# Kernel tuning notes

Measured on AMD Instinct MI355X. Metric: run time of the kernel, lower is better.

The kernel has to match this reference:

```python
import jax, jax.numpy as jnp
import numpy as np

NI = 256  # channels (c)
EPS = 1e-5  # BatchNorm eps


def setup_inputs() -> dict:
    key = jax.random.key(0)
    ks = jax.random.split(key, 7)
    n, c, h, w = 8, NI, 96, 96
    inp = jax.random.normal(ks[0], (n, c, h, w), dtype=jnp.float32)
    bn_gamma = jnp.ones((c,), dtype=jnp.float32)
    bn_beta = jnp.zeros((c,), dtype=jnp.float32)
    s_qkv = 1.0 / np.sqrt(c)
    w_qkv = jax.random.uniform(ks[1], (c, 3 * c), dtype=jnp.float32, minval=-s_qkv, maxval=s_qkv)
    b_qkv = jax.random.uniform(ks[2], (3 * c,), dtype=jnp.float32, minval=-s_qkv, maxval=s_qkv)
    w_proj = jax.random.uniform(ks[3], (c, c), dtype=jnp.float32, minval=-s_qkv, maxval=s_qkv)
    b_proj = jax.random.uniform(ks[4], (c,), dtype=jnp.float32, minval=-s_qkv, maxval=s_qkv)
    return {"inp": inp, "bn_gamma": bn_gamma, "bn_beta": bn_beta,
            "w_qkv": w_qkv, "b_qkv": b_qkv, "w_proj": w_proj, "b_proj": b_proj}


def reference(inp, bn_gamma, bn_beta, w_qkv, b_qkv, w_proj, b_proj):
    n, c, h, w = inp.shape
    # BatchNorm2d (training-mode batch statistics, biased variance)
    mean = jnp.mean(inp, axis=(0, 2, 3), keepdims=True)
    var = jnp.var(inp, axis=(0, 2, 3), keepdims=True)
    xn = (inp - mean) * jax.lax.rsqrt(var + EPS)
    xn = xn * bn_gamma.reshape(1, c, 1, 1) + bn_beta.reshape(1, c, 1, 1)
    # (n, c, h*w) -> (n, s, c)
    x = jnp.transpose(xn.reshape(n, c, h * w), (0, 2, 1))
    # fused QKV projection: (n, s, 3c)
    qkv = x @ w_qkv + b_qkv
    q, k, v = jnp.split(qkv, 3, axis=-1)  # each (n, s, c); nheads=1
    # linear attention: v + q @ (k^T @ v), avoids the (s, s) score matrix
    kv = jnp.einsum('nsd,nse->nde', k, v)        # (n, c, c)
    attn = v + jnp.einsum('nsd,nde->nse', q, kv)  # (n, s, c)
    # output projection (dropout is identity in eval mode)
    y = attn @ w_proj + b_proj                    # (n, s, c)
    y = jnp.transpose(y, (0, 2, 1)).reshape(n, c, h, w)
    return y + inp
```

## Files before the change

kernel.cpp:

```cpp
#include <hip/hip_runtime.h>
#include <hip/hip_bf16.h>
#include <stdint.h>

#define S 9216
#define C 256
#define NB 8
#define EPS 1e-5f
#define LDST 40
#define GSPL 18
#define GLD 144

typedef __attribute__((ext_vector_type(8))) short bf16x8;
typedef __attribute__((ext_vector_type(4))) float f32x4;
typedef unsigned short u16;
typedef unsigned int u32;

#define WS_SC   0
#define WS_RX   4096
#define WS_DS   16384
#define WS_U    20480
#define WS_PV   32768
#define WS_P1   45056
#define WS_CZ   49152
#define WS_WKT  65536
#define WS_WPT  196608
#define WS_WPV  327680
#define WS_GB   458752
#define WS_T1   1507328
#define WS_AC2  2555904
#define WS_M    3604480
#define WS_P    4718592

__device__ __forceinline__ float bf2f(u16 b) { return __uint_as_float((u32)b << 16); }
__device__ __forceinline__ u16 cvt1(float x) {
    __hip_bfloat16 h = __float2bfloat16(x);
    return *(u16*)&h;
}
__device__ __forceinline__ bf16x8 pack8(float4 a, float4 b) {
    union { bf16x8 v; u16 h[8]; } u;
    u.h[0] = cvt1(a.x); u.h[1] = cvt1(a.y); u.h[2] = cvt1(a.z); u.h[3] = cvt1(a.w);
    u.h[4] = cvt1(b.x); u.h[5] = cvt1(b.y); u.h[6] = cvt1(b.z); u.h[7] = cvt1(b.w);
    return u.v;
}
__device__ __forceinline__ void tile_enum(int tile, int& ti, int& tj) {
    if (tile < 4) { ti = tile; tj = tile; }
    else {
        const int u = tile - 4;
        ti = (u < 3) ? 0 : ((u < 5) ? 1 : 2);
        tj = (u < 3) ? (u + 1) : ((u < 5) ? (u - 1) : 3);
    }
}

__global__ __launch_bounds__(256)
void wt_build(const float* __restrict__ w_qkv, const float* __restrict__ w_proj,
              u16* __restrict__ wkT, u16* __restrict__ wpT) {
    const int r0 = blockIdx.x, c = threadIdx.x;
    if (r0 < 256) {
        wkT[(size_t)r0 * 256 + c] = cvt1(w_qkv[(size_t)c * 768 + 256 + r0]);
    } else {
        const int o = r0 - 256;
        wpT[(size_t)o * 256 + c] = cvt1(w_proj[(size_t)c * 256 + o]);
    }
}

__global__ __launch_bounds__(256)
void wpv_gemm(const u16* __restrict__ wpT, const float* __restrict__ w_qkv,
              u16* __restrict__ Wpv) {
    const int bid = blockIdx.x;
    const int ot = bid >> 2, ct = bid & 3;
    const int tid = threadIdx.x;
    const int w = tid >> 6, l = tid & 63, g = l >> 4, r = l & 15;
    const int wr = w >> 1, wc = w & 1;
    const int mb = ot * 64 + wr * 32, nb = ct * 64 + wc * 32;

    f32x4 acc[2][2];
    #pragma unroll
    for (int i = 0; i < 2; ++i)
        #pragma unroll
        for (int j = 0; j < 2; ++j) acc[i][j] = (f32x4){0.f, 0.f, 0.f, 0.f};

    for (int k0 = 0; k0 < 256; k0 += 32) {
        bf16x8 a[2], b[2];
        #pragma unroll
        for (int i = 0; i < 2; ++i)
            a[i] = *(const bf16x8*)&wpT[(size_t)(mb + i * 16 + r) * 256 + k0 + g * 8];
        #pragma unroll
        for (int j = 0; j < 2; ++j) {
            const float* p = w_qkv + (size_t)(nb + j * 16 + r) * 768 + 512 + k0 + g * 8;
            b[j] = pack8(*(const float4*)p, *(const float4*)(p + 4));
        }
        #pragma unroll
        for (int i = 0; i < 2; ++i)
            #pragma unroll
            for (int j = 0; j < 2; ++j)
                acc[i][j] = __builtin_amdgcn_mfma_f32_16x16x32_bf16(a[i], b[j], acc[i][j], 0, 0, 0);
    }
    #pragma unroll
    for (int i = 0; i < 2; ++i)
        #pragma unroll
        for (int q = 0; q < 4; ++q) {
            const int row = mb + i * 16 + g * 4 + q;
            #pragma unroll
            for (int j = 0; j < 2; ++j)
                Wpv[(size_t)row * 256 + nb + j * 16 + r] = cvt1(acc[i][j][q]);
        }
}

__global__ __launch_bounds__(256)
void gram_part(const float* __restrict__ inp, float* __restrict__ P, float* __restrict__ rx) {
    __shared__ u16 Lsm[128 * GLD];
    const int bid = blockIdx.x;
    const int wid = (bid & 7) * 180 + (bid >> 3);
    const int z = wid / 180;
    const int rem = wid % 180;
    const int tile = rem / GSPL;
    const int sp = rem % GSPL;
    int ti, tj; tile_enum(tile, ti, tj);
    const bool diag = (ti == tj);

    const int tid = threadIdx.x;
    const int w = tid >> 6, l = tid & 63;
    const int g = l >> 4, r = l & 15;
    const int wr = w >> 1, wc = w & 1;

    const float* Abase = inp + ((size_t)(z * C + ti * 64)) * S;
    const float* Bbase = inp + ((size_t)(z * C + tj * 64)) * S;

    f32x4 acc[2][2];
    #pragma unroll
    for (int i = 0; i < 2; ++i)
        #pragma unroll
        for (int j = 0; j < 2; ++j) acc[i][j] = (f32x4){0.f, 0.f, 0.f, 0.f};
    float rsA[16];
    #pragma unroll
    for (int rr = 0; rr < 16; ++rr) rsA[rr] = 0.f;

    const int sbeg = sp * 512;
    for (int it = 0; it < 4; ++it) {
        const int s0 = sbeg + it * 128;
        __syncthreads();
        #pragma unroll
        for (int rr = 0; rr < 16; ++rr) {
            const int row = w * 16 + rr;
            float2 f = *(const float2*)&Abase[(size_t)row * S + s0 + l * 2];
            u32 pk = (u32)cvt1(f.x) | ((u32)cvt1(f.y) << 16);
            *(u32*)&Lsm[row * GLD + l * 2] = pk;
            if (diag) {
                float rs = f.x + f.y;
                rs += __shfl_xor(rs, 1);  rs += __shfl_xor(rs, 2);
                rs += __shfl_xor(rs, 4);  rs += __shfl_xor(rs, 8);
                rs += __shfl_xor(rs, 16); rs += __shfl_xor(rs, 32);
                rsA[rr] += rs;
            }
        }
        if (!diag) {
            #pragma unroll
            for (int rr = 0; rr < 16; ++rr) {
                const int row = w * 16 + rr;
                float2 f = *(const float2*)&Bbase[(size_t)row * S + s0 + l * 2];
                u32 pk = (u32)cvt1(f.x) | ((u32)cvt1(f.y) << 16);
                *(u32*)&Lsm[(64 + row) * GLD + l * 2] = pk;
            }
        }
        __syncthreads();
        const int bb = diag ? 0 : 64;
        #pragma unroll
        for (int k0 = 0; k0 < 128; k0 += 32) {
            bf16x8 a[2], b[2];
            #pragma unroll
            for (int i = 0; i < 2; ++i)
                a[i] = *(const bf16x8*)&Lsm[(wr * 32 + i * 16 + r) * GLD + k0 + g * 8];
            #pragma unroll
            for (int j = 0; j < 2; ++j)
                b[j] = *(const bf16x8*)&Lsm[(bb + wc * 32 + j * 16 + r) * GLD + k0 + g * 8];
            #pragma unroll
            for (int i = 0; i < 2; ++i)
                #pragma unroll
                for (int j = 0; j < 2; ++j)
                    acc[i][j] = __builtin_amdgcn_mfma_f32_16x16x32_bf16(a[i], b[j], acc[i][j], 0, 0, 0);
        }
    }
    float* PP = P + (((size_t)(z * 10 + tile) * GSPL + sp) << 12);
    #pragma unroll
    for (int i = 0; i < 2; ++i)
        #pragma unroll
        for (int q = 0; q < 4; ++q) {
            const int row = wr * 32 + i * 16 + g * 4 + q;
            #pragma unroll
            for (int j = 0; j < 2; ++j)
                PP[row * 64 + wc * 32 + j * 16 + r] = acc[i][j][q];
        }
    if (diag && l == 0) {
        #pragma unroll
        for (int rr = 0; rr < 16; ++rr)
            atomicAdd(&rx[z * 256 + ti * 64 + w * 16 + rr], rsA[rr]);
    }
}

__global__ __launch_bounds__(256)
void red_diag(const float* __restrict__ P, float* __restrict__ diagS) {
    const int c = threadIdx.x;
    const int pp = blockIdx.x;
    float s = 0.f;
    #pragma unroll
    for (int k = 0; k < 4; ++k) {
        const int pair = pp * 4 + k;
        const int zz = pair / GSPL, sp2 = pair % GSPL;
        s += P[(((size_t)(zz * 10 + (c >> 6)) * GSPL + sp2) << 12) + (size_t)(c & 63) * 65];
    }
    atomicAdd(&diagS[c], s);
}

__global__ __launch_bounds__(256)
void bn_fin(const float* __restrict__ diagS, const float* __restrict__ rx,
            const float* __restrict__ gamma, const float* __restrict__ beta,
            float* __restrict__ sc_sh) {
    const int c = threadIdx.x;
    float s = 0.f;
    #pragma unroll
    for (int z = 0; z < NB; ++z) s += rx[z * 256 + c];
    const float q = diagS[c];
    const float invN = 1.0f / (float)(NB * S);
    float m = s * invN;
    float var = q * invN - m * m;
    float rstd = rsqrtf(var + EPS);
    float sc = gamma[c] * rstd;
    sc_sh[c] = sc;
    sc_sh[C + c] = beta[c] - m * sc;
}

__global__ __launch_bounds__(256)
void prep_g2(const float* __restrict__ P, const float* __restrict__ rx,
             const float* __restrict__ sc_sh, u16* __restrict__ Gb) {
    __shared__ float scs[256], shs[256], rxl[256];
    __shared__ u16 T[64][66];
    const int bid = blockIdx.x;
    const int z = bid / 10, tile = bid % 10;
    int ti, tj; tile_enum(tile, ti, tj);
    const int t = threadIdx.x;
    scs[t] = sc_sh[t]; shs[t] = sc_sh[C + t]; rxl[t] = rx[z * 256 + t];
    __syncthreads();
    const int rr = t >> 2, cc = (t & 3) * 16;
    float s[16];
    #pragma unroll
    for (int e = 0; e < 16; ++e) s[e] = 0.f;
    for (int sp = 0; sp < GSPL; ++sp) {
        const float* src = P + (((size_t)(z * 10 + tile) * GSPL + sp) << 12) + rr * 64 + cc;
        #pragma unroll
        for (int e4 = 0; e4 < 4; ++e4) {
            float4 v = *(const float4*)&src[e4 * 4];
            s[e4 * 4 + 0] += v.x; s[e4 * 4 + 1] += v.y;
            s[e4 * 4 + 2] += v.z; s[e4 * 4 + 3] += v.w;
        }
    }
    const int gr = ti * 64 + rr;
    u16 o[16];
    #pragma unroll
    for (int e = 0; e < 16; ++e) {
        const int gc = tj * 64 + cc + e;
        float v = scs[gr] * scs[gc] * s[e] + scs[gr] * shs[gc] * rxl[gr]
                + shs[gr] * scs[gc] * rxl[gc] + 9216.f * shs[gr] * shs[gc];
        o[e] = cvt1(v);
    }
    u16* dst = Gb + (size_t)z * 65536 + (size_t)gr * 256 + tj * 64 + cc;
    *(uint4*)&dst[0] = *(uint4*)&o[0];
    *(uint4*)&dst[8] = *(uint4*)&o[8];
    if (ti != tj) {
        #pragma unroll
        for (int e = 0; e < 16; ++e) T[rr][cc + e] = o[e];
        __syncthreads();
        u16 o2[16];
        #pragma unroll
        for (int e = 0; e < 16; ++e) o2[e] = T[cc + e][rr];
        u16* dst2 = Gb + (size_t)z * 65536 + (size_t)(tj * 64 + rr) * 256 + ti * 64 + cc;
        *(uint4*)&dst2[0] = *(uint4*)&o2[0];
        *(uint4*)&dst2[8] = *(uint4*)&o2[8];
    }
}

__global__ __launch_bounds__(256)
void prep_v(const float* __restrict__ sc_sh, const float* __restrict__ rx,
            const u16* __restrict__ wkT, const u16* __restrict__ Wpv,
            const u16* __restrict__ wpT, const float* __restrict__ b_qkv,
            float* __restrict__ uvec, float* __restrict__ pvec, float* __restrict__ p1) {
    const int z = blockIdx.x, t = threadIdx.x;
    __shared__ float rsn[256], bvl[256];
    rsn[t] = sc_sh[t] * rx[z * 256 + t] + 9216.f * sc_sh[C + t];
    bvl[t] = b_qkv[512 + t];
    __syncthreads();
    float au = 0.f, ap = 0.f;
    const u16* krow = wkT + (size_t)t * 256;
    const u16* prow = Wpv + (size_t)t * 256;
    for (int cb = 0; cb < 256; cb += 8) {
        uint4 kp = *(const uint4*)&krow[cb];
        uint4 pp = *(const uint4*)&prow[cb];
        const u16* kk = (const u16*)&kp;
        const u16* qq = (const u16*)&pp;
        #pragma unroll
        for (int u = 0; u < 8; ++u) {
            au = fmaf(bf2f(kk[u]), rsn[cb + u], au);
            ap = fmaf(bf2f(qq[u]), rsn[cb + u], ap);
        }
    }
    uvec[z * 256 + t] = au;
    pvec[z * 256 + t] = ap;
    if (z == 0) {
        float a1 = 0.f;
        const u16* wrow = wpT + (size_t)t * 256;
        for (int cb = 0; cb < 256; cb += 8) {
            uint4 wp = *(const uint4*)&wrow[cb];
            const u16* ww = (const u16*)&wp;
            #pragma unroll
            for (int u = 0; u < 8; ++u) a1 = fmaf(bf2f(ww[u]), bvl[cb + u], a1);
        }
        p1[t] = a1;
    }
}

__global__ __launch_bounds__(256)
void t1_gemm(const u16* __restrict__ Wpv, const u16* __restrict__ Gb,
             u16* __restrict__ T1) {
    const int bid = blockIdx.x;
    const int wid = (bid & 7) * 16 + (bid >> 3);
    const int z = wid >> 4, ot = (wid >> 2) & 3, ct = wid & 3;
    const int tid = threadIdx.x;
    const int w = tid >> 6, l = tid & 63, g = l >> 4, r = l & 15;
    const int wr = w >> 1, wc = w & 1;
    const int mb = ot * 64 + wr * 32, nb = ct * 64 + wc * 32;
    const u16* Gz = Gb + (size_t)z * 65536;

    f32x4 acc[2][2];
    #pragma unroll
    for (int i = 0; i < 2; ++i)
        #pragma unroll
        for (int j = 0; j < 2; ++j) acc[i][j] = (f32x4){0.f, 0.f, 0.f, 0.f};

    for (int k0 = 0; k0 < 256; k0 += 32) {
        bf16x8 a[2], b[2];
        #pragma unroll
        for (int i = 0; i < 2; ++i)
            a[i] = *(const bf16x8*)&Wpv[(size_t)(mb + i * 16 + r) * 256 + k0 + g * 8];
        #pragma unroll
        for (int j = 0; j < 2; ++j)
            b[j] = *(const bf16x8*)&Gz[(size_t)(nb + j * 16 + r) * 256 + k0 + g * 8];
        #pragma unroll
        for (int i = 0; i < 2; ++i)
            #pragma unroll
            for (int j = 0; j < 2; ++j)
                acc[i][j] = __builtin_amdgcn_mfma_f32_16x16x32_bf16(a[i], b[j], acc[i][j], 0, 0, 0);
    }
    u16* Tz = T1 + (size_t)z * 65536;
    #pragma unroll
    for (int i = 0; i < 2; ++i)
        #pragma unroll
        for (int q = 0; q < 4; ++q) {
            const int row = mb + i * 16 + g * 4 + q;
            #pragma unroll
            for (int j = 0; j < 2; ++j)
                Tz[(size_t)row * 256 + nb + j * 16 + r] = cvt1(acc[i][j][q]);
        }
}

__global__ __launch_bounds__(256)
void ac2_gemm(const u16* __restrict__ T1, const u16* __restrict__ wkT,
              const float* __restrict__ uvec, const float* __restrict__ pvec,
              const float* __restrict__ p1, const float* __restrict__ b_qkv,
              u16* __restrict__ Ac2) {
    const int bid = blockIdx.x;
    const int wid = (bid & 7) * 16 + (bid >> 3);
    const int z = wid >> 4, ot = (wid >> 2) & 3, ct = wid & 3;
    const int tid = threadIdx.x;
    const int w = tid >> 6, l = tid & 63, g = l >> 4, r = l & 15;
    const int wr = w >> 1, wc = w & 1;
    const int mb = ot * 64 + wr * 32, nb = ct * 64 + wc * 32;
    const u16* Tz = T1 + (size_t)z * 65536;

    f32x4 acc[2][2];
    #pragma unroll
    for (int i = 0; i < 2; ++i)
        #pragma unroll
        for (int j = 0; j < 2; ++j) acc[i][j] = (f32x4){0.f, 0.f, 0.f, 0.f};

    for (int k0 = 0; k0 < 256; k0 += 32) {
        bf16x8 a[2], b[2];
        #pragma unroll
        for (int i = 0; i < 2; ++i)
            a[i] = *(const bf16x8*)&Tz[(size_t)(mb + i * 16 + r) * 256 + k0 + g * 8];
        #pragma unroll
        for (int j = 0; j < 2; ++j)
            b[j] = *(const bf16x8*)&wkT[(size_t)(nb + j * 16 + r) * 256 + k0 + g * 8];
        #pragma unroll
        for (int i = 0; i < 2; ++i)
            #pragma unroll
            for (int j = 0; j < 2; ++j)
                acc[i][j] = __builtin_amdgcn_mfma_f32_16x16x32_bf16(a[i], b[j], acc[i][j], 0, 0, 0);
    }
    u16* Az = Ac2 + (size_t)z * 65536;
    #pragma unroll
    for (int i = 0; i < 2; ++i)
        #pragma unroll
        for (int q = 0; q < 4; ++q) {
            const int row = mb + i * 16 + g * 4 + q;
            const float p1r = p1[row];
            const float pvr = pvec[z * 256 + row];
            #pragma unroll
            for (int j = 0; j < 2; ++j) {
                const int col = nb + j * 16 + r;
                const float bkv = b_qkv[256 + col];
                const float uv = uvec[z * 256 + col];
                float v = acc[i][j][q] + p1r * (uv + 9216.f * bkv) + pvr * bkv;
                Az[(size_t)row * 256 + col] = cvt1(v);
            }
        }
}

__global__ __launch_bounds__(256)
void m_gemm(const u16* __restrict__ Ac2, const float* __restrict__ w_qkv,
            const u16* __restrict__ Wpv, const float* __restrict__ p1,
            const float* __restrict__ b_qkv, const float* __restrict__ b_proj,
            u16* __restrict__ M, float* __restrict__ constz) {
    const int bid = blockIdx.x;
    const int wid = (bid & 7) * 16 + (bid >> 3);
    const int z = wid >> 4, ot = (wid >> 2) & 3, ct = wid & 3;
    const int tid = threadIdx.x;
    const int w = tid >> 6, l = tid & 63, g = l >> 4, r = l & 15;
    const int wr = w >> 1, wc = w & 1;
    const int mb = ot * 64 + wr * 32, nb = ct * 64 + wc * 32;
    const u16* Az = Ac2 + (size_t)z * 65536;
    const bool docz = (wc == 0 && ct == 0);

    f32x4 acc[2][2];
    #pragma unroll
    for (int i = 0; i < 2; ++i)
        #pragma unroll
        for (int j = 0; j < 2; ++j) acc[i][j] = (f32x4){0.f, 0.f, 0.f, 0.f};
    float cacc[2] = {0.f, 0.f};

    for (int k0 = 0; k0 < 256; k0 += 32) {
        bf16x8 a[2], b[2];
        #pragma unroll
        for (int i = 0; i < 2; ++i)
            a[i] = *(const bf16x8*)&Az[(size_t)(mb + i * 16 + r) * 256 + k0 + g * 8];
        #pragma unroll
        for (int j = 0; j < 2; ++j) {
            const float* p = w_qkv + (size_t)(nb + j * 16 + r) * 768 + k0 + g * 8;
            b[j] = pack8(*(const float4*)p, *(const float4*)(p + 4));
        }
        if (docz) {
            float4 q0 = *(const float4*)&b_qkv[k0 + g * 8];
            float4 q1 = *(const float4*)&b_qkv[k0 + g * 8 + 4];
            float bqv[8] = {q0.x, q0.y, q0.z, q0.w, q1.x, q1.y, q1.z, q1.w};
            #pragma unroll
            for (int i = 0; i < 2; ++i) {
                bf16x8 av = a[i];
                #pragma unroll
                for (int u = 0; u < 8; ++u)
                    cacc[i] = fmaf(bf2f((u16)av[u]), bqv[u], cacc[i]);
            }
        }
        #pragma unroll
        for (int i = 0; i < 2; ++i)
            #pragma unroll
            for (int j = 0; j < 2; ++j)
                acc[i][j] = __builtin_amdgcn_mfma_f32_16x16x32_bf16(a[i], b[j], acc[i][j], 0, 0, 0);
    }
    u16* Mz = M + (size_t)z * 65536;
    #pragma unroll
    for (int i = 0; i < 2; ++i)
        #pragma unroll
        for (int q = 0; q < 4; ++q) {
            const int row = mb + i * 16 + g * 4 + q;
            #pragma unroll
            for (int j = 0; j < 2; ++j) {
                const int col = nb + j * 16 + r;
                float v = acc[i][j][q] + bf2f(Wpv[(size_t)row * 256 + col]);
                Mz[(size_t)row * 256 + col] = cvt1(v);
            }
        }
    if (docz) {
        #pragma unroll
        for (int i = 0; i < 2; ++i) {
            float rr = cacc[i];
            rr += __shfl_xor(rr, 16, 64);
            rr += __shfl_xor(rr, 32, 64);
            if (l < 16) {
                const int o = mb + i * 16 + l;
                constz[z * 256 + o] = b_proj[o] + p1[o] + rr;
            }
        }
    }
}

__global__ __launch_bounds__(256)
void out_gemm(const u16* __restrict__ M, const float* __restrict__ inp,
              const float* __restrict__ sc_sh, const float* __restrict__ constz,
              float* __restrict__ out) {
    __shared__ u16 Bsm[128 * LDST];
    const int bid = blockIdx.x;
    const int wid = (bid & 7) * 144 + (bid >> 3);
    const int ot = wid & 1;
    const int st = (wid >> 1) % 72;
    const int z  = wid / 144;

    const int tid = threadIdx.x;
    const int l = tid & 63, w = tid >> 6;
    const int m0 = (w >> 1) * 64, n0 = (w & 1) * 64;
    const int g = l >> 4, r = l & 15;
    const int rowL = tid & 127;
    const int half = (tid >> 7) * 16;

    const u16* Mrow = M + (size_t)z * 65536 + (size_t)(ot * 128) * 256;
    const float* inpz = inp + (size_t)z * C * S + (size_t)st * 128 + rowL;

    f32x4 acc[4][4];
    #pragma unroll
    for (int i = 0; i < 4; ++i)
        #pragma unroll
        for (int j = 0; j < 4; ++j) acc[i][j] = (f32x4){0.f, 0.f, 0.f, 0.f};

    for (int k0 = 0; k0 < 256; k0 += 32) {
        {
            u32 pk[8];
            #pragma unroll
            for (int u = 0; u < 8; ++u) {
                const int c = k0 + half + u * 2;
                float x0 = inpz[(size_t)c * S];
                float x1 = inpz[(size_t)(c + 1) * S];
                u16 b0 = cvt1(fmaf(x0, sc_sh[c], sc_sh[C + c]));
                u16 b1 = cvt1(fmaf(x1, sc_sh[c + 1], sc_sh[C + c + 1]));
                pk[u] = (u32)b0 | ((u32)b1 << 16);
            }
            uint4 q0, q1;
            q0.x = pk[0]; q0.y = pk[1]; q0.z = pk[2]; q0.w = pk[3];
            q1.x = pk[4]; q1.y = pk[5]; q1.z = pk[6]; q1.w = pk[7];
            *(uint4*)&Bsm[rowL * LDST + half] = q0;
            *(uint4*)&Bsm[rowL * LDST + half + 8] = q1;
        }
        __syncthreads();
        bf16x8 a[4], b[4];
        #pragma unroll
        for (int i = 0; i < 4; ++i)
            a[i] = *(const bf16x8*)&Mrow[(size_t)(m0 + i * 16 + r) * 256 + k0 + g * 8];
        #pragma unroll
        for (int j = 0; j < 4; ++j) b[j] = *(const bf16x8*)&Bsm[(n0 + j * 16 + r) * LDST + g * 8];
        #pragma unroll
        for (int i = 0; i < 4; ++i)
            #pragma unroll
            for (int j = 0; j < 4; ++j)
                acc[i][j] = __builtin_amdgcn_mfma_f32_16x16x32_bf16(a[i], b[j], acc[i][j], 0, 0, 0);
        __syncthreads();
    }
    #pragma unroll
    for (int i = 0; i < 4; ++i) {
        #pragma unroll
        for (int q = 0; q < 4; ++q) {
            const int o = ot * 128 + m0 + i * 16 + g * 4 + q;
            const float cz = constz[z * 256 + o];
            const size_t base = ((size_t)z * C + o) * S + st * 128;
            #pragma unroll
            for (int j = 0; j < 4; ++j) {
                const int sl = n0 + j * 16 + r;
                out[base + sl] = acc[i][j][q] + cz + inp[base + sl];
            }
        }
    }
}

extern "C" void kernel_launch(void* const* d_in, const int* in_sizes, int n_in,
                              void* d_out, int out_size, void* d_ws, size_t ws_size,
                              hipStream_t stream) {
    const float* inp    = (const float*)d_in[0];
    const float* gamma  = (const float*)d_in[1];
    const float* beta   = (const float*)d_in[2];
    const float* w_qkv  = (const float*)d_in[3];
    const float* b_qkv  = (const float*)d_in[4];
    const float* w_proj = (const float*)d_in[5];
    const float* b_proj = (const float*)d_in[6];
    float* out = (float*)d_out;

    char* ws = (char*)d_ws;
    float* sc_sh = (float*)(ws + WS_SC);
    float* rx    = (float*)(ws + WS_RX);
    float* diagS = (float*)(ws + WS_DS);
    float* uvec  = (float*)(ws + WS_U);
    float* pvec  = (float*)(ws + WS_PV);
    float* p1    = (float*)(ws + WS_P1);
    float* cz    = (float*)(ws + WS_CZ);
    u16*   wkT   = (u16*)(ws + WS_WKT);
    u16*   wpT   = (u16*)(ws + WS_WPT);
    u16*   Wpv   = (u16*)(ws + WS_WPV);
    u16*   Gb    = (u16*)(ws + WS_GB);
    u16*   T1    = (u16*)(ws + WS_T1);
    u16*   Ac2   = (u16*)(ws + WS_AC2);
    u16*   Mm    = (u16*)(ws + WS_M);
    float* P     = (float*)(ws + WS_P);

    hipMemsetAsync(rx, 0, NB * 256 * sizeof(float), stream);
    hipMemsetAsync(diagS, 0, 256 * sizeof(float), stream);

    wt_build<<<dim3(512), dim3(256), 0, stream>>>(w_qkv, w_proj, wkT, wpT);
    wpv_gemm<<<dim3(16), dim3(256), 0, stream>>>(wpT, w_qkv, Wpv);
    gram_part<<<dim3(1440), dim3(256), 0, stream>>>(inp, P, rx);
    red_diag<<<dim3(36), dim3(256), 0, stream>>>(P, diagS);
    bn_fin<<<dim3(1), dim3(256), 0, stream>>>(diagS, rx, gamma, beta, sc_sh);
    prep_g2<<<dim3(80), dim3(256), 0, stream>>>(P, rx, sc_sh, Gb);
    prep_v<<<dim3(NB), dim3(256), 0, stream>>>(sc_sh, rx, wkT, Wpv, wpT, b_qkv, uvec, pvec, p1);
    t1_gemm<<<dim3(128), dim3(256), 0, stream>>>(Wpv, Gb, T1);
    ac2_gemm<<<dim3(128), dim3(256), 0, stream>>>(T1, wkT, uvec, pvec, p1, b_qkv, Ac2);
    m_gemm<<<dim3(128), dim3(256), 0, stream>>>(Ac2, w_qkv, Wpv, p1, b_qkv, b_proj, Mm, cz);
    out_gemm<<<dim3(1152), dim3(256), 0, stream>>>(Mm, inp, sc_sh, cz, out);
}
```

Before: 194.2 us.

## Pre-convert input to bf16 (plain and transposed) and fold BN into M

A new cvt pass reads the fp32 input once and writes it as bf16 in both channel-major and spatial-major layouts, computing per-channel sums and sums of squares on the way. The Gram kernel then streams bf16 directly from global memory in 128x128 tiles without LDS, and out_gemm reads pre-transposed bf16 activations with no LDS staging. The BN scale is folded into M and the BN shift into extra bias vectors (pw, shw). This removes repeated fp32 reads and conversions inside the GEMMs, but adds about 75 MB of bf16 workspace traffic. Statistics are now taken from bf16-rounded values, which slightly changes precision.

```diff
diff --git a/kernel.cpp b/kernel.cpp
--- a/kernel.cpp
+++ b/kernel.cpp
@@ -6,9 +6,6 @@
 #define C 256
 #define NB 8
 #define EPS 1e-5f
-#define LDST 40
-#define GSPL 18
-#define GLD 144
 
 typedef __attribute__((ext_vector_type(8))) short bf16x8;
 typedef __attribute__((ext_vector_type(4))) float f32x4;
@@ -19,9 +16,11 @@
 #define WS_RX   4096
 #define WS_DS   16384
 #define WS_U    20480
-#define WS_PV   32768
+#define WS_PV2  32768
 #define WS_P1   45056
-#define WS_CZ   49152
+#define WS_PW   49152
+#define WS_SHW  53248
+#define WS_CZ   57344
 #define WS_WKT  65536
 #define WS_WPT  196608
 #define WS_WPV  327680
@@ -29,7 +28,9 @@
 #define WS_T1   1507328
 #define WS_AC2  2555904
 #define WS_M    3604480
-#define WS_P    4718592
+#define WS_XB   5242880
+#define WS_XBT  42991616
+#define WS_P    80740352
 
 __device__ __forceinline__ float bf2f(u16 b) { return __uint_as_float((u32)b << 16); }
 __device__ __forceinline__ u16 cvt1(float x) {
@@ -41,14 +42,6 @@
     u.h[0] = cvt1(a.x); u.h[1] = cvt1(a.y); u.h[2] = cvt1(a.z); u.h[3] = cvt1(a.w);
     u.h[4] = cvt1(b.x); u.h[5] = cvt1(b.y); u.h[6] = cvt1(b.z); u.h[7] = cvt1(b.w);
     return u.v;
-}
-__device__ __forceinline__ void tile_enum(int tile, int& ti, int& tj) {
-    if (tile < 4) { ti = tile; tj = tile; }
-    else {
-        const int u = tile - 4;
-        ti = (u < 3) ? 0 : ((u < 5) ? 1 : 2);
-        tj = (u < 3) ? (u + 1) : ((u < 5) ? (u - 1) : 3);
-    }
 }
 
 __global__ __launch_bounds__(256)
@@ -107,108 +100,46 @@
 }
 
 __global__ __launch_bounds__(256)
-void gram_part(const float* __restrict__ inp, float* __restrict__ P, float* __restrict__ rx) {
-    __shared__ u16 Lsm[128 * GLD];
-    const int bid = blockIdx.x;
-    const int wid = (bid & 7) * 180 + (bid >> 3);
-    const int z = wid / 180;
-    const int rem = wid % 180;
-    const int tile = rem / GSPL;
-    const int sp = rem % GSPL;
-    int ti, tj; tile_enum(tile, ti, tj);
-    const bool diag = (ti == tj);
-
-    const int tid = threadIdx.x;
-    const int w = tid >> 6, l = tid & 63;
-    const int g = l >> 4, r = l & 15;
-    const int wr = w >> 1, wc = w & 1;
-
-    const float* Abase = inp + ((size_t)(z * C + ti * 64)) * S;
-    const float* Bbase = inp + ((size_t)(z * C + tj * 64)) * S;
-
-    f32x4 acc[2][2];
-    #pragma unroll
-    for (int i = 0; i < 2; ++i)
-        #pragma unroll
-        for (int j = 0; j < 2; ++j) acc[i][j] = (f32x4){0.f, 0.f, 0.f, 0.f};
-    float rsA[16];
-    #pragma unroll
-    for (int rr = 0; rr < 16; ++rr) rsA[rr] = 0.f;
-
-    const int sbeg = sp * 512;
-    for (int it = 0; it < 4; ++it) {
-        const int s0 = sbeg + it * 128;
-        __syncthreads();
-        #pragma unroll
-        for (int rr = 0; rr < 16; ++rr) {
-            const int row = w * 16 + rr;
-            float2 f = *(const float2*)&Abase[(size_t)row * S + s0 + l * 2];
-            u32 pk = (u32)cvt1(f.x) | ((u32)cvt1(f.y) << 16);
-            *(u32*)&Lsm[row * GLD + l * 2] = pk;
-            if (diag) {
-                float rs = f.x + f.y;
-                rs += __shfl_xor(rs, 1);  rs += __shfl_xor(rs, 2);
-                rs += __shfl_xor(rs, 4);  rs += __shfl_xor(rs, 8);
-                rs += __shfl_xor(rs, 16); rs += __shfl_xor(rs, 32);
-                rsA[rr] += rs;
-            }
-        }
-        if (!diag) {
-            #pragma unroll
-            for (int rr = 0; rr < 16; ++rr) {
-                const int row = w * 16 + rr;
-                float2 f = *(const float2*)&Bbase[(size_t)row * S + s0 + l * 2];
-                u32 pk = (u32)cvt1(f.x) | ((u32)cvt1(f.y) << 16);
-                *(u32*)&Lsm[(64 + row) * GLD + l * 2] = pk;
-            }
-        }
-        __syncthreads();
-        const int bb = diag ? 0 : 64;
-        #pragma unroll
-        for (int k0 = 0; k0 < 128; k0 += 32) {
-            bf16x8 a[2], b[2];
-            #pragma unroll
-            for (int i = 0; i < 2; ++i)
-                a[i] = *(const bf16x8*)&Lsm[(wr * 32 + i * 16 + r) * GLD + k0 + g * 8];
-            #pragma unroll
-            for (int j = 0; j < 2; ++j)
-                b[j] = *(const bf16x8*)&Lsm[(bb + wc * 32 + j * 16 + r) * GLD + k0 + g * 8];
-            #pragma unroll
-            for (int i = 0; i < 2; ++i)
-                #pragma unroll
-                for (int j = 0; j < 2; ++j)
-                    acc[i][j] = __builtin_amdgcn_mfma_f32_16x16x32_bf16(a[i], b[j], acc[i][j], 0, 0, 0);
-        }
-    }
-    float* PP = P + (((size_t)(z * 10 + tile) * GSPL + sp) << 12);
-    #pragma unroll
-    for (int i = 0; i < 2; ++i)
-        #pragma unroll
-        for (int q = 0; q < 4; ++q) {
-            const int row = wr * 32 + i * 16 + g * 4 + q;
-            #pragma unroll
-            for (int j = 0; j < 2; ++j)
-                PP[row * 64 + wc * 32 + j * 16 + r] = acc[i][j][q];
-        }
-    if (diag && l == 0) {
-        #pragma unroll
-        for (int rr = 0; rr < 16; ++rr)
-            atomicAdd(&rx[z * 256 + ti * 64 + w * 16 + rr], rsA[rr]);
-    }
-}
-
-__global__ __launch_bounds__(256)
-void red_diag(const float* __restrict__ P, float* __restrict__ diagS) {
-    const int c = threadIdx.x;
-    const int pp = blockIdx.x;
-    float s = 0.f;
-    #pragma unroll
-    for (int k = 0; k < 4; ++k) {
-        const int pair = pp * 4 + k;
-        const int zz = pair / GSPL, sp2 = pair % GSPL;
-        s += P[(((size_t)(zz * 10 + (c >> 6)) * GSPL + sp2) << 12) + (size_t)(c & 63) * 65];
-    }
-    atomicAdd(&diagS[c], s);
+void cvt(const float* __restrict__ inp, u16* __restrict__ xb, u16* __restrict__ xbT,
+         float* __restrict__ rx, float* __restrict__ diagS) {
+    __shared__ u16 T[64 * 258];
+    const int bid = blockIdx.x;
+    const int z = bid / 144, sb = bid % 144;
+    const int s0 = sb * 64;
+    const int t = threadIdx.x;
+    const int lane = t & 63, w = t >> 6;
+
+    for (int it = 0; it < 64; ++it) {
+        const int row = it * 4 + w;
+        const size_t gidx = ((size_t)(z * C + row)) * S + s0 + lane;
+        float v = inp[gidx];
+        u16 b = cvt1(v);
+        xb[gidx] = b;
+        T[lane * 258 + row] = b;
+    }
+    __syncthreads();
+    {
+        float sum = 0.f, ssq = 0.f;
+        #pragma unroll 8
+        for (int sl = 0; sl < 64; ++sl) {
+            float v = bf2f(T[sl * 258 + t]);
+            sum += v; ssq = fmaf(v, v, ssq);
+        }
+        atomicAdd(&rx[z * 256 + t], sum);
+        atomicAdd(&diagS[t], ssq);
+    }
+    const int sl = t >> 2, q4 = t & 3;
+    u16* dst = xbT + ((size_t)z * S + s0 + sl) * 256 + q4 * 64;
+    const u16* src = &T[sl * 258 + q4 * 64];
+    #pragma unroll
+    for (int k = 0; k < 8; ++k) {
+        u32 a0 = *(const u32*)&src[k * 8 + 0];
+        u32 a1 = *(const u32*)&src[k * 8 + 2];
+        u32 a2 = *(const u32*)&src[k * 8 + 4];
+        u32 a3 = *(const u32*)&src[k * 8 + 6];
+        uint4 q; q.x = a0; q.y = a1; q.z = a2; q.w = a3;
+        *(uint4*)&dst[k * 8] = q;
+    }
 }
 
 __global__ __launch_bounds__(256)
@@ -230,65 +161,119 @@
 }
 
 __global__ __launch_bounds__(256)
+void gram(const u16* __restrict__ xb, float* __restrict__ P) {
+    const int bid = blockIdx.x;
+    const int wid = (bid & 7) * 48 + (bid >> 3);
+    const int z = wid / 48;
+    const int rem = wid % 48;
+    const int tile = rem >> 4;
+    const int sp = rem & 15;
+    const int ti = (tile == 1) ? 1 : 0;
+    const int tj = (tile == 0) ? 0 : 1;
+
+    const int t = threadIdx.x;
+    const int w = t >> 6, l = t & 63, g = l >> 4, r = l & 15;
+    const int wr = w >> 1, wc = w & 1;
+
+    const u16* Az = xb + (size_t)z * C * S;
+    const u16* Ab = Az + (size_t)(ti * 128 + wr * 64) * S;
+    const u16* Bb = Az + (size_t)(tj * 128 + wc * 64) * S;
+
+    f32x4 acc[4][4];
+    #pragma unroll
+    for (int i = 0; i < 4; ++i)
+        #pragma unroll
+        for (int j = 0; j < 4; ++j) acc[i][j] = (f32x4){0.f, 0.f, 0.f, 0.f};
+
+    const int sbeg = sp * 576;
+    for (int k0 = 0; k0 < 576; k0 += 32) {
+        const int scol = sbeg + k0 + g * 8;
+        bf16x8 a[4], b[4];
+        #pragma unroll
+        for (int i = 0; i < 4; ++i)
+            a[i] = *(const bf16x8*)&Ab[(size_t)(i * 16 + r) * S + scol];
+        #pragma unroll
+        for (int j = 0; j < 4; ++j)
+            b[j] = *(const bf16x8*)&Bb[(size_t)(j * 16 + r) * S + scol];
+        #pragma unroll
+        for (int i = 0; i < 4; ++i)
+            #pragma unroll
+            for (int j = 0; j < 4; ++j)
+                acc[i][j] = __builtin_amdgcn_mfma_f32_16x16x32_bf16(a[i], b[j], acc[i][j], 0, 0, 0);
+    }
+    float* PP = P + (((size_t)(z * 3 + tile) * 16 + sp) << 14);
+    #pragma unroll
+    for (int i = 0; i < 4; ++i)
+        #pragma unroll
+        for (int q = 0; q < 4; ++q) {
+            const int row = wr * 64 + i * 16 + g * 4 + q;
+            #pragma unroll
+            for (int j = 0; j < 4; ++j)
+                PP[row * 128 + wc * 64 + j * 16 + r] = acc[i][j][q];
+        }
+}
+
+__global__ __launch_bounds__(256)
 void prep_g2(const float* __restrict__ P, const float* __restrict__ rx,
              const float* __restrict__ sc_sh, u16* __restrict__ Gb) {
     __shared__ float scs[256], shs[256], rxl[256];
-    __shared__ u16 T[64][66];
-    const int bid = blockIdx.x;
-    const int z = bid / 10, tile = bid % 10;
-    int ti, tj; tile_enum(tile, ti, tj);
+    const int bid = blockIdx.x;
+    const int z = bid / 3, tile = bid % 3;
+    const int ti = (tile == 1) ? 1 : 0;
+    const int tj = (tile == 0) ? 0 : 1;
     const int t = threadIdx.x;
     scs[t] = sc_sh[t]; shs[t] = sc_sh[C + t]; rxl[t] = rx[z * 256 + t];
     __syncthreads();
-    const int rr = t >> 2, cc = (t & 3) * 16;
-    float s[16];
-    #pragma unroll
-    for (int e = 0; e < 16; ++e) s[e] = 0.f;
-    for (int sp = 0; sp < GSPL; ++sp) {
-        const float* src = P + (((size_t)(z * 10 + tile) * GSPL + sp) << 12) + rr * 64 + cc;
-        #pragma unroll
-        for (int e4 = 0; e4 < 4; ++e4) {
+    const int rr = t >> 1, cc0 = (t & 1) * 64;
+    float s[64];
+    #pragma unroll
+    for (int e = 0; e < 64; ++e) s[e] = 0.f;
+    for (int sp = 0; sp < 16; ++sp) {
+        const float* src = P + (((size_t)(z * 3 + tile) * 16 + sp) << 14) + rr * 128 + cc0;
+        #pragma unroll
+        for (int e4 = 0; e4 < 16; ++e4) {
             float4 v = *(const float4*)&src[e4 * 4];
             s[e4 * 4 + 0] += v.x; s[e4 * 4 + 1] += v.y;
             s[e4 * 4 + 2] += v.z; s[e4 * 4 + 3] += v.w;
         }
     }
-    const int gr = ti * 64 + rr;
-    u16 o[16];
-    #pragma unroll
-    for (int e = 0; e < 16; ++e) {
-        const int gc = tj * 64 + cc + e;
-        float v = scs[gr] * scs[gc] * s[e] + scs[gr] * shs[gc] * rxl[gr]
-                + shs[gr] * scs[gc] * rxl[gc] + 9216.f * shs[gr] * shs[gc];
+    const int gr = ti * 128 + rr;
+    const float scr = scs[gr], shr = shs[gr], rxr = rxl[gr];
+    u16 o[64];
+    #pragma unroll
+    for (int e = 0; e < 64; ++e) {
+        const int gc = tj * 128 + cc0 + e;
+        float v = scr * scs[gc] * s[e] + scr * shs[gc] * rxr
+                + shr * scs[gc] * rxl[gc] + 9216.f * shr * shs[gc];
         o[e] = cvt1(v);
     }
-    u16* dst = Gb + (size_t)z * 65536 + (size_t)gr * 256 + tj * 64 + cc;
-    *(uint4*)&dst[0] = *(uint4*)&o[0];
-    *(uint4*)&dst[8] = *(uint4*)&o[8];
+    u16* Gz = Gb + (size_t)z * 65536;
+    u16* dst = Gz + (size_t)gr * 256 + tj * 128 + cc0;
+    #pragma unroll
+    for (int k = 0; k < 8; ++k) *(uint4*)&dst[k * 8] = *(uint4*)&o[k * 8];
     if (ti != tj) {
         #pragma unroll
-        for (int e = 0; e < 16; ++e) T[rr][cc + e] = o[e];
-        __syncthreads();
-        u16 o2[16];
-        #pragma unroll
-        for (int e = 0; e < 16; ++e) o2[e] = T[cc + e][rr];
-        u16* dst2 = Gb + (size_t)z * 65536 + (size_t)(tj * 64 + rr) * 256 + ti * 64 + cc;
-        *(uint4*)&dst2[0] = *(uint4*)&o2[0];
-        *(uint4*)&dst2[8] = *(uint4*)&o2[8];
+        for (int e = 0; e < 64; ++e) {
+            const int gc = tj * 128 + cc0 + e;
+            Gz[(size_t)gc * 256 + ti * 128 + rr] = o[e];
+        }
     }
 }
 
 __global__ __launch_bounds__(256)
 void prep_v(const float* __restrict__ sc_sh, const float* __restrict__ rx,
             const u16* __restrict__ wkT, const u16* __restrict__ Wpv,
-            const u16* __restrict__ wpT, const float* __restrict__ b_qkv,
-            float* __restrict__ uvec, float* __restrict__ pvec, float* __restrict__ p1) {
+            const u16* __restrict__ wpT, const float* __restrict__ w_qkv,
+            const float* __restrict__ b_qkv,
+            float* __restrict__ uvec, float* __restrict__ pvec,
+            float* __restrict__ p1, float* __restrict__ pw, float* __restrict__ shw) {
     const int z = blockIdx.x, t = threadIdx.x;
-    __shared__ float rsn[256], bvl[256];
+    __shared__ float rsn[256], bvl[256], shl[256];
     rsn[t] = sc_sh[t] * rx[z * 256 + t] + 9216.f * sc_sh[C + t];
     bvl[t] = b_qkv[512 + t];
+    shl[t] = sc_sh[C + t];
     __syncthreads();
-    float au = 0.f, ap = 0.f;
+    float au = 0.f, ap = 0.f, apw = 0.f;
     const u16* krow = wkT + (size_t)t * 256;
     const u16* prow = Wpv + (size_t)t * 256;
     for (int cb = 0; cb < 256; cb += 8) {
@@ -299,13 +284,15 @@
         #pragma unroll
         for (int u = 0; u < 8; ++u) {
             au = fmaf(bf2f(kk[u]), rsn[cb + u], au);
-            ap = fmaf(bf2f(qq[u]), rsn[cb + u], ap);
+            float pv = bf2f(qq[u]);
+            ap = fmaf(pv, rsn[cb + u], ap);
+            apw = fmaf(pv, shl[cb + u], apw);
         }
     }
     uvec[z * 256 + t] = au;
     pvec[z * 256 + t] = ap;
     if (z == 0) {
-        float a1 = 0.f;
+        float a1 = 0.f, asw = 0.f;
         const u16* wrow = wpT + (size_t)t * 256;
         for (int cb = 0; cb < 256; cb += 8) {
             uint4 wp = *(const uint4*)&wrow[cb];
@@ -313,8 +300,14 @@
             #pragma unroll
             for (int u = 0; u < 8; ++u) a1 = fmaf(bf2f(ww[u]), bvl[cb + u], a1);
         }
+        for (int c = 0; c < 256; ++c)
+            asw = fmaf(w_qkv[(size_t)c * 768 + t], shl[c], asw);
         p1[t] = a1;
-    }
+        pw[t] = apw;
+        shw[t] = asw;
+    } else if (t == 0) {
+    }
+    if (z == 0) {  } else if (z == 1 && t < 0) { }
 }
 
 __global__ __launch_bounds__(256)
@@ -417,7 +410,9 @@
 __global__ __launch_bounds__(256)
 void m_gemm(const u16* __restrict__ Ac2, const float* __restrict__ w_qkv,
             const u16* __restrict__ Wpv, const float* __restrict__ p1,
+            const float* __restrict__ pw, const float* __restrict__ shw,
             const float* __restrict__ b_qkv, const float* __restrict__ b_proj,
+            const float* __restrict__ sc_sh,
             u16* __restrict__ M, float* __restrict__ constz) {
     const int bid = blockIdx.x;
     const int wid = (bid & 7) * 16 + (bid >> 3);
@@ -447,9 +442,12 @@
             b[j] = pack8(*(const float4*)p, *(const float4*)(p + 4));
         }
         if (docz) {
-            float4 q0 = *(const float4*)&b_qkv[k0 + g * 8];
-            float4 q1 = *(const float4*)&b_qkv[k0 + g * 8 + 4];
-            float bqv[8] = {q0.x, q0.y, q0.z, q0.w, q1.x, q1.y, q1.z, q1.w};
+            float bqv[8];
+            #pragma unroll
+            for (int u = 0; u < 8; ++u) {
+                const int kg = k0 + g * 8 + u;
+                bqv[u] = b_qkv[kg] + shw[kg];
+            }
             #pragma unroll
             for (int i = 0; i < 2; ++i) {
                 bf16x8 av = a[i];
@@ -474,92 +472,67 @@
             for (int j = 0; j < 2; ++j) {
                 const int col = nb + j * 16 + r;
                 float v = acc[i][j][q] + bf2f(Wpv[(size_t)row * 256 + col]);
-                Mz[(size_t)row * 256 + col] = cvt1(v);
+                Mz[(size_t)row * 256 + col] = cvt1(v * sc_sh[col]);
             }
         }
     if (docz) {
         #pragma unroll
         for (int i = 0; i < 2; ++i) {
-            float rr = cacc[i];
-            rr += __shfl_xor(rr, 16, 64);
-            rr += __shfl_xor(rr, 32, 64);
+            float rr2 = cacc[i];
+            rr2 += __shfl_xor(rr2, 16, 64);
+            rr2 += __shfl_xor(rr2, 32, 64);
             if (l < 16) {
                 const int o = mb + i * 16 + l;
-                constz[z * 256 + o] = b_proj[o] + p1[o] + rr;
+                constz[z * 256 + o] = b_proj[o] + p1[o] + pw[o] + rr2;
             }
         }
     }
 }
 
 __global__ __launch_bounds__(256)
-void out_gemm(const u16* __restrict__ M, const float* __restrict__ inp,
-              const float* __restrict__ sc_sh, const float* __restrict__ constz,
+void out_gemm(const u16* __restrict__ M, const u16* __restrict__ xbT,
+              const float* __restrict__ inp, const float* __restrict__ constz,
               float* __restrict__ out) {
-    __shared__ u16 Bsm[128 * LDST];
-    const int bid = blockIdx.x;
-    const int wid = (bid & 7) * 144 + (bid >> 3);
-    const int ot = wid & 1;
-    const int st = (wid >> 1) % 72;
-    const int z  = wid / 144;
-
-    const int tid = threadIdx.x;
-    const int l = tid & 63, w = tid >> 6;
-    const int m0 = (w >> 1) * 64, n0 = (w & 1) * 64;
-    const int g = l >> 4, r = l & 15;
-    const int rowL = tid & 127;
-    const int half = (tid >> 7) * 16;
-
-    const u16* Mrow = M + (size_t)z * 65536 + (size_t)(ot * 128) * 256;
-    const float* inpz = inp + (size_t)z * C * S + (size_t)st * 128 + rowL;
-
-    f32x4 acc[4][4];
-    #pragma unroll
-    for (int i = 0; i < 4; ++i)
+    const int bid = blockIdx.x;
+    const int wid = (bid & 7) * 72 + (bid >> 3);
+    const int z = wid / 72, st = wid % 72;
+    const int t = threadIdx.x;
+    const int w = t >> 6, l = t & 63, g = l >> 4, r = l & 15;
+    const int wo = w >> 1, wsb = w & 1;
+
+    const u16* Mz = M + (size_t)z * 65536 + (size_t)(wo * 128) * 256;
+    const u16* Bz = xbT + ((size_t)z * S + st * 128 + wsb * 64) * 256;
+
+    f32x4 acc[8][4];
+    #pragma unroll
+    for (int i = 0; i < 8; ++i)
         #pragma unroll
         for (int j = 0; j < 4; ++j) acc[i][j] = (f32x4){0.f, 0.f, 0.f, 0.f};
 
     for (int k0 = 0; k0 < 256; k0 += 32) {
-        {
-            u32 pk[8];
-            #pragma unroll
-            for (int u = 0; u < 8; ++u) {
-                const int c = k0 + half + u * 2;
-                float x0 = inpz[(size_t)c * S];
-                float x1 = inpz[(size_t)(c + 1) * S];
-                u16 b0 = cvt1(fmaf(x0, sc_sh[c], sc_sh[C + c]));
-                u16 b1 = cvt1(fmaf(x1, sc_sh[c + 1], sc_sh[C + c + 1]));
-                pk[u] = (u32)b0 | ((u32)b1 << 16);
-            }
-            uint4 q0, q1;
-            q0.x = pk[0]; q0.y = pk[1]; q0.z = pk[2]; q0.w = pk[3];
-            q1.x = pk[4]; q1.y = pk[5]; q1.z = pk[6]; q1.w = pk[7];
-            *(uint4*)&Bsm[rowL * LDST + half] = q0;
-            *(uint4*)&Bsm[rowL * LDST + half + 8] = q1;
-        }
-        __syncthreads();
-        bf16x8 a[4], b[4];
-        #pragma unroll
-        for (int i = 0; i < 4; ++i)
-            a[i] = *(const bf16x8*)&Mrow[(size_t)(m0 + i * 16 + r) * 256 + k0 + g * 8];
-        #pragma unroll
-        for (int j = 0; j < 4; ++j) b[j] = *(const bf16x8*)&Bsm[(n0 + j * 16 + r) * LDST + g * 8];
-        #pragma unroll
-        for (int i = 0; i < 4; ++i)
+        bf16x8 a[8], b[4];
+        #pragma unroll
+        for (int i = 0; i < 8; ++i)
+            a[i] = *(const bf16x8*)&Mz[(size_t)(i * 16 + r) * 256 + k0 + g * 8];
+        #pragma unroll
+        for (int j = 0; j < 4; ++j)
+            b[j] = *(const bf16x8*)&Bz[(size_t)(j * 16 + r) * 256 + k0 + g * 8];
+        #pragma unroll
+        for (int i = 0; i < 8; ++i)
             #pragma unroll
             for (int j = 0; j < 4; ++j)
                 acc[i][j] = __builtin_amdgcn_mfma_f32_16x16x32_bf16(a[i], b[j], acc[i][j], 0, 0, 0);
-        __syncthreads();
-    }
-    #pragma unroll
-    for (int i = 0; i < 4; ++i) {
+    }
+    #pragma unroll
+    for (int i = 0; i < 8; ++i) {
         #pragma unroll
         for (int q = 0; q < 4; ++q) {
-            const int o = ot * 128 + m0 + i * 16 + g * 4 + q;
+            const int o = wo * 128 + i * 16 + g * 4 + q;
             const float cz = constz[z * 256 + o];
-            const size_t base = ((size_t)z * C + o) * S + st * 128;
+            const size_t base = ((size_t)(z * C + o)) * S + st * 128 + wsb * 64;
             #pragma unroll
             for (int j = 0; j < 4; ++j) {
-                const int sl = n0 + j * 16 + r;
+                const int sl = j * 16 + r;
                 out[base + sl] = acc[i][j][q] + cz + inp[base + sl];
             }
         }
@@ -583,8 +556,10 @@
     float* rx    = (float*)(ws + WS_RX);
     float* diagS = (float*)(ws + WS_DS);
     float* uvec  = (float*)(ws + WS_U);
-    float* pvec  = (float*)(ws + WS_PV);
+    float* pvec  = (float*)(ws + WS_PV2);
     float* p1    = (float*)(ws + WS_P1);
+    float* pw    = (float*)(ws + WS_PW);
+    float* shw   = (float*)(ws + WS_SHW);
     float* cz    = (float*)(ws + WS_CZ);
     u16*   wkT   = (u16*)(ws + WS_WKT);
     u16*   wpT   = (u16*)(ws + WS_WPT);
@@ -593,6 +568,8 @@
     u16*   T1    = (u16*)(ws + WS_T1);
     u16*   Ac2   = (u16*)(ws + WS_AC2);
     u16*   Mm    = (u16*)(ws + WS_M);
+    u16*   xb    = (u16*)(ws + WS_XB);
+    u16*   xbT   = (u16*)(ws + WS_XBT);
     float* P     = (float*)(ws + WS_P);
 
     hipMemsetAsync(rx, 0, NB * 256 * sizeof(float), stream);
@@ -600,13 +577,15 @@
 
     wt_build<<<dim3(512), dim3(256), 0, stream>>>(w_qkv, w_proj, wkT, wpT);
     wpv_gemm<<<dim3(16), dim3(256), 0, stream>>>(wpT, w_qkv, Wpv);
-    gram_part<<<dim3(1440), dim3(256), 0, stream>>>(inp, P, rx);
-    red_diag<<<dim3(36), dim3(256), 0, stream>>>(P, diagS);
+    cvt<<<dim3(1152), dim3(256), 0, stream>>>(inp, xb, xbT, rx, diagS);
     bn_fin<<<dim3(1), dim3(256), 0, stream>>>(diagS, rx, gamma, beta, sc_sh);
-    prep_g2<<<dim3(80), dim3(256), 0, stream>>>(P, rx, sc_sh, Gb);
-    prep_v<<<dim3(NB), dim3(256), 0, stream>>>(sc_sh, rx, wkT, Wpv, wpT, b_qkv, uvec, pvec, p1);
+    gram<<<dim3(384), dim3(256), 0, stream>>>(xb, P);
+    prep_g2<<<dim3(24), dim3(256), 0, stream>>>(P, rx, sc_sh, Gb);
+    prep_v<<<dim3(NB), dim3(256), 0, stream>>>(sc_sh, rx, wkT, Wpv, wpT, w_qkv, b_qkv,
+                                               uvec, pvec, p1, pw, shw);
     t1_gemm<<<dim3(128), dim3(256), 0, stream>>>(Wpv, Gb, T1);
     ac2_gemm<<<dim3(128), dim3(256), 0, stream>>>(T1, wkT, uvec, pvec, p1, b_qkv, Ac2);
-    m_gemm<<<dim3(128), dim3(256), 0, stream>>>(Ac2, w_qkv, Wpv, p1, b_qkv, b_proj, Mm, cz);
-    out_gemm<<<dim3(1152), dim3(256), 0, stream>>>(Mm, inp, sc_sh, cz, out);
-}
+    m_gemm<<<dim3(128), dim3(256), 0, stream>>>(Ac2, w_qkv, Wpv, p1, pw, shw,
+                                                b_qkv, b_proj, sc_sh, Mm, cz);
+    out_gemm<<<dim3(576), dim3(256), 0, stream>>>(Mm, xbT, inp, cz, out);
+}
```

Measured after the change: 258.6 us. 33.2% more time.
